# Optimization experiments

Hardware: AMD Instinct MI355X
Metric: run time of the kernel (lower is better)

The kernel has to match this reference:

```python
import jax, jax.numpy as jnp
import numpy as np

DIM_IN = 1024
DIM_Q = 1024
DIM_K = 1024
DIM_V = 1024
HEADS = 16

def setup_inputs() -> dict:
    key = jax.random.key(0)
    ks = jax.random.split(key, 5)
    s = 1.0 / np.sqrt(DIM_IN)
    return {
        "x": jax.random.normal(ks[0], (2, 2048, DIM_IN), dtype=jnp.float32),
        "Wq": jax.random.uniform(ks[1], (DIM_IN, DIM_Q), jnp.float32, -s, s),
        "Wk": jax.random.uniform(ks[2], (DIM_IN, DIM_K), jnp.float32, -s, s),
        "Wv": jax.random.uniform(ks[3], (DIM_IN, DIM_V), jnp.float32, -s, s),
        "Wo": jax.random.uniform(ks[4], (DIM_V, DIM_V), jnp.float32, -1.0/np.sqrt(DIM_V), 1.0/np.sqrt(DIM_V)),
    }

def reference(x, Wq, Wk, Wv, Wo):
    B, S, _ = x.shape
    H = HEADS
    q = (x @ Wq).reshape(B, S, H, DIM_Q // H).transpose(0, 2, 1, 3)  # [B,H,S,dq]
    k = (x @ Wk).reshape(B, S, H, DIM_K // H).transpose(0, 2, 1, 3)
    v = (x @ Wv).reshape(B, S, H, DIM_V // H).transpose(0, 2, 1, 3)
    scores = jnp.einsum("bhsd,bhtd->bhst", q, k)  # no pre-softmax scaling (as in source)
    # NOTE: source divides by sqrt(dim_q) AFTER softmax — replicated faithfully.
    attn = jax.nn.softmax(scores, axis=-1) / jnp.sqrt(jnp.float32(DIM_Q))
    out = jnp.einsum("bhst,bhtd->bhsd", attn, v)  # [B,H,S,dv]
    out = out.transpose(0, 2, 1, 3).reshape(B, S, DIM_V)
    return out @ Wo
```

## Files before the change

### kernel.cpp

```cpp
#include <hip/hip_runtime.h>
#include <hip/hip_bf16.h>


typedef __attribute__((ext_vector_type(8))) short bf16x8;
typedef __attribute__((ext_vector_type(4))) short short4v;
typedef __attribute__((ext_vector_type(4))) float f32x4;

typedef const __attribute__((address_space(1))) void gvoid_t;
typedef __attribute__((address_space(3))) void svoid_t;
#define GLDS16(g, l) \
  __builtin_amdgcn_global_load_lds((gvoid_t*)(g), (svoid_t*)(l), 16, 0, 0)

#define MFMA16(a, b, c) __builtin_amdgcn_mfma_f32_16x16x32_bf16((a), (b), (c), 0, 0, 0)

#if defined(__has_builtin)
#if __has_builtin(__builtin_amdgcn_exp2f)
#define EXP2(x) __builtin_amdgcn_exp2f(x)
#else
#define EXP2(x) exp2f(x)
#endif
#else
#define EXP2(x) exp2f(x)
#endif

#define LOG2E 1.4426950408889634f
#define NSHIFT 17.312340490667561f

static __device__ __forceinline__ short f2bf(float f) {
  __hip_bfloat16 h = __float2bfloat16(f);
  short s;
  __builtin_memcpy(&s, &h, 2);
  return s;
}

static __device__ __forceinline__ unsigned pack2bf(float lo, float hi) {
  float2 t; t.x = lo; t.y = hi;
  __hip_bfloat162 h2 = __float22bfloat162_rn(t);
  unsigned u;
  __builtin_memcpy(&u, &h2, 4);
  return u;
}

__global__ __launch_bounds__(256) void prep(const float* __restrict__ x,
                                            const float* __restrict__ Wq,
                                            const float* __restrict__ Wk,
                                            const float* __restrict__ Wv,
                                            const float* __restrict__ Wo,
                                            short* __restrict__ xb,
                                            short* __restrict__ wqkvt,
                                            short* __restrict__ wot) {
  __shared__ float tile[64][65];
  int bid = blockIdx.x;
  int tid = threadIdx.x;
  if (bid < 2048) {
    int i = bid * 256 + tid;
    const float4* p = (const float4*)(x + (size_t)i * 8);
    float4 a = p[0], b = p[1];
    bf16x8 o;
    o[0] = f2bf(a.x); o[1] = f2bf(a.y); o[2] = f2bf(a.z); o[3] = f2bf(a.w);
    o[4] = f2bf(b.x); o[5] = f2bf(b.y); o[6] = f2bf(b.z); o[7] = f2bf(b.w);
    *(bf16x8*)(xb + (size_t)i * 8) = o;
    return;
  }
  bid -= 2048;
  int mat = bid >> 8;
  int t = bid & 255;
  int tn = (t & 15) * 64;
  int tk = (t >> 4) * 64;
  const float* src = (mat == 0) ? Wq : (mat == 1) ? Wk : (mat == 2) ? Wv : Wo;
  short* dst = (mat < 3) ? (wqkvt + (size_t)mat * 1024 * 1024) : wot;

  int c4 = (tid & 15) * 4;
#pragma unroll
  for (int it = 0; it < 4; ++it) {
    int r = (tid >> 4) + it * 16;
    float4 v = *(const float4*)(src + (size_t)(tk + r) * 1024 + tn + c4);
    tile[r][c4 + 0] = v.x; tile[r][c4 + 1] = v.y;
    tile[r][c4 + 2] = v.z; tile[r][c4 + 3] = v.w;
  }
  __syncthreads();
  int n = tid >> 2;
  int kc = (tid & 3) * 16;
  bf16x8 o0, o1;
#pragma unroll
  for (int j = 0; j < 8; ++j) {
    o0[j] = f2bf(tile[kc + j][n]);
    o1[j] = f2bf(tile[kc + 8 + j][n]);
  }
  *(bf16x8*)(dst + (size_t)(tn + n) * 1024 + tk + kc) = o0;
  *(bf16x8*)(dst + (size_t)(tn + n) * 1024 + tk + kc + 8) = o1;
}

__global__ __launch_bounds__(256, 2) void gemm_qkv(const short* __restrict__ A,
                                                   const short* __restrict__ Bt,
                                                   short* __restrict__ qk,
                                                   short* __restrict__ vt) {
  constexpr int K = 1024;
  __shared__ short As[2][128 * 64];
  __shared__ short Bs[2][192 * 64];
  const int tid = threadIdx.x;
  const int lane = tid & 63;
  const int w = tid >> 6;
  const int lr = lane & 15, lg = lane >> 4;
  const int bid = blockIdx.x;
  const int orig = (bid & 7) * 64 + (bid >> 3);
  const int m0 = (orig >> 4) * 128, n0 = (orig & 15) * 192;
  const int wm = (w >> 1) * 64, wn = (w & 1) * 96;

  auto stage = [&](int kt, int bb) {
#pragma unroll
    for (int it = 0; it < 4; ++it) {
      int id = it * 256 + tid;
      int row = id >> 3, c = id & 7;
      int sc = c ^ (row & 7);
      GLDS16(A + (size_t)(m0 + row) * K + kt + sc * 8, &As[bb][0] + id * 8);
    }
#pragma unroll
    for (int it = 0; it < 6; ++it) {
      int id = it * 256 + tid;
      int row = id >> 3, c = id & 7;
      int sc = c ^ (row & 7);
      GLDS16(Bt + (size_t)(n0 + row) * K + kt + sc * 8, &Bs[bb][0] + id * 8);
    }
  };

  f32x4 acc[4][6] = {};

  stage(0, 0);
  __syncthreads();

  int cur = 0;
  for (int kt = 0; kt < K; kt += 64) {
    if (kt + 64 < K) stage(kt + 64, cur ^ 1);
    const short* Ab = &As[cur][0];
    const short* Bb = &Bs[cur][0];
#pragma unroll
    for (int kk2 = 0; kk2 < 2; ++kk2) {
      int cw = kk2 * 4 + lg;
      bf16x8 bfr[6];
#pragma unroll
      for (int ni = 0; ni < 6; ++ni) {
        int row = wn + ni * 16 + lr;
        bfr[ni] = *(const bf16x8*)(Bb + row * 64 + ((cw ^ (row & 7)) * 8));
      }
      __builtin_amdgcn_s_setprio(1);
#pragma unroll
      for (int mi = 0; mi < 4; ++mi) {
        int row = wm + mi * 16 + lr;
        bf16x8 af = *(const bf16x8*)(Ab + row * 64 + ((cw ^ (row & 7)) * 8));
#pragma unroll
        for (int ni = 0; ni < 6; ++ni)
          acc[mi][ni] = MFMA16(af, bfr[ni], acc[mi][ni]);
      }
      __builtin_amdgcn_s_setprio(0);
    }
    __syncthreads();
    cur ^= 1;
  }

#pragma unroll
  for (int mi = 0; mi < 4; ++mi) {
#pragma unroll
    for (int ni = 0; ni < 6; ++ni) {
      int m = m0 + wm + mi * 16 + lg * 4;
      int n = n0 + wn + ni * 16 + lr;
      if (n < 2048) {
        float sc = (n < 1024) ? LOG2E : 1.0f;
#pragma unroll
        for (int r = 0; r < 4; ++r)
          qk[(size_t)(m + r) * 2048 + n] = f2bf(acc[mi][ni][r] * sc);
      } else {
        int nv = n - 2048;
        int vtrow = ((m >> 11) * 16 + (nv >> 6)) * 64 + (nv & 63);
        int scol = m & 2047;
        int psc = (scol & ~31) | ((scol & 0xC) << 1) | ((scol & 16) >> 2) |
                  (scol & 3);
        short4v pv;
#pragma unroll
        for (int r = 0; r < 4; ++r) pv[r] = f2bf(acc[mi][ni][r]);
        *(short4v*)(vt + (size_t)vtrow * 2048 + psc) = pv;
      }
    }
  }
}

__global__ __launch_bounds__(256) void gemm_out(const short* __restrict__ A,
                                                const short* __restrict__ Bt,
                                                float* __restrict__ C) {
  constexpr int K = 1024, N = 1024;
  __shared__ short As[2][128 * 64];
  __shared__ short Bs[2][64 * 64];
  const int tid = threadIdx.x;
  const int lane = tid & 63;
  const int w = tid >> 6;
  const int lr = lane & 15, lg = lane >> 4;
  const int bid = blockIdx.x;
  const int orig = (bid & 7) * 64 + (bid >> 3);
  const int m0 = (orig >> 4) * 128, n0 = (orig & 15) * 64;
  const int wm = (w >> 1) * 64, wn = (w & 1) * 32;

  auto stage = [&](int kt, int bb) {
#pragma unroll
    for (int it = 0; it < 4; ++it) {
      int id = it * 256 + tid;
      int row = id >> 3, c = id & 7;
      int sc = c ^ (row & 7);
      GLDS16(A + (size_t)(m0 + row) * K + kt + sc * 8, &As[bb][0] + id * 8);
    }
#pragma unroll
    for (int it = 0; it < 2; ++it) {
      int id = it * 256 + tid;
      int row = id >> 3, c = id & 7;
      int sc = c ^ (row & 7);
      GLDS16(Bt + (size_t)(n0 + row) * K + kt + sc * 8, &Bs[bb][0] + id * 8);
    }
  };

  f32x4 acc[4][2] = {};

  stage(0, 0);
  __syncthreads();

  int cur = 0;
  for (int kt = 0; kt < K; kt += 64) {
    if (kt + 64 < K) stage(kt + 64, cur ^ 1);
    const short* Ab = &As[cur][0];
    const short* Bb = &Bs[cur][0];
#pragma unroll
    for (int kk2 = 0; kk2 < 2; ++kk2) {
      int cw = kk2 * 4 + lg;
      bf16x8 bfr[2];
#pragma unroll
      for (int ni = 0; ni < 2; ++ni) {
        int row = wn + ni * 16 + lr;
        bfr[ni] = *(const bf16x8*)(Bb + row * 64 + ((cw ^ (row & 7)) * 8));
      }
      __builtin_amdgcn_s_setprio(1);
#pragma unroll
      for (int mi = 0; mi < 4; ++mi) {
        int row = wm + mi * 16 + lr;
        bf16x8 af = *(const bf16x8*)(Ab + row * 64 + ((cw ^ (row & 7)) * 8));
#pragma unroll
        for (int ni = 0; ni < 2; ++ni)
          acc[mi][ni] = MFMA16(af, bfr[ni], acc[mi][ni]);
      }
      __builtin_amdgcn_s_setprio(0);
    }
    __syncthreads();
    cur ^= 1;
  }

#pragma unroll
  for (int mi = 0; mi < 4; ++mi) {
#pragma unroll
    for (int ni = 0; ni < 2; ++ni) {
      int m = m0 + wm + mi * 16 + lg * 4;
      int n = n0 + wn + ni * 16 + lr;
#pragma unroll
      for (int r = 0; r < 4; ++r) C[(size_t)(m + r) * N + n] = acc[mi][ni][r];
    }
  }
}

__global__ __launch_bounds__(256, 2) void attn_fwd(const short* __restrict__ qk,
                                                   const short* __restrict__ vt,
                                                   short* __restrict__ outb) {
  constexpr int S = 2048, LDQ = 2048;
  constexpr int NT = S / 128;
  const int fid = blockIdx.x;
  const int xcd = fid & 7, j = fid >> 3;
  const int qt = j & 15;
  const int pair = xcd * 4 + (j >> 4);
  const int h = pair & 15, b = pair >> 4;

  const int tid = threadIdx.x, lane = tid & 63, w = tid >> 6;
  const int lr = lane & 15, lg = lane >> 4;
  const int s7 = lr & 7;
  const int qb = qt * 128 + w * 32;

  __shared__ short Ks[2][128][64];
  __shared__ short Vs[2][64][128];

  const short* base = qk + (size_t)b * S * LDQ + h * 64;
  const short* vbase = vt + (size_t)(b * 16 + h) * 64 * 2048;

  bf16x8 qA0 = *(const bf16x8*)(base + (size_t)(qb + lr) * LDQ + lg * 8);
  bf16x8 qA1 = *(const bf16x8*)(base + (size_t)(qb + lr) * LDQ + 32 + lg * 8);
  bf16x8 qB0 = *(const bf16x8*)(base + (size_t)(qb + 16 + lr) * LDQ + lg * 8);
  bf16x8 qB1 = *(const bf16x8*)(base + (size_t)(qb + 16 + lr) * LDQ + 32 + lg * 8);

  bf16x8 ones;
#pragma unroll
  for (int i = 0; i < 8; ++i) ones[i] = (short)0x3F80;

  auto stageK = [&](int kt, int bb) {
#pragma unroll
    for (int it = 0; it < 4; ++it) {
      int id = it * 256 + tid;
      int row = id >> 3, c = id & 7;
      int sc = c ^ (row & 7);
      GLDS16(base + 1024 + (size_t)(kt + row) * LDQ + sc * 8,
             &Ks[bb][0][0] + id * 8);
    }
  };
  auto stageV = [&](int kt, int bb) {
#pragma unroll
    for (int it = 0; it < 4; ++it) {
      int id = it * 256 + tid;
      int row = id >> 4, c = id & 15;
      int sc = c ^ (row & 15);
      GLDS16(vbase + (size_t)row * 2048 + kt + sc * 8,
             &Vs[bb][0][0] + id * 8);
    }
  };

  f32x4 oA[4] = {}, oB[4] = {};
  f32x4 laccA = {}, laccB = {};
  bf16x8 pA[4], pB[4];

  stageK(0, 0);
  __syncthreads();

  for (int t = 0; t < NT; ++t) {
    const int cb = t & 1;
    if (t + 1 < NT) stageK((t + 1) * 128, cb ^ 1);
    stageV(t * 128, cb);

    const short* Kb = &Ks[cb][0][0];

    f32x4 sA[8], sB[8];
    __builtin_amdgcn_s_setprio(1);
#pragma unroll
    for (int kc = 0; kc < 8; ++kc) {
      int krow = kc * 16 + lr;
      bf16x8 kf0 = *(const bf16x8*)(Kb + krow * 64 + ((lg ^ s7) * 8));
      bf16x8 kf1 = *(const bf16x8*)(Kb + krow * 64 + (((4 + lg) ^ s7) * 8));
      f32x4 s = {-NSHIFT, -NSHIFT, -NSHIFT, -NSHIFT};
      s = MFMA16(kf0, qA0, s);
      s = MFMA16(kf1, qA1, s);
      sA[kc] = s;
      f32x4 u = {-NSHIFT, -NSHIFT, -NSHIFT, -NSHIFT};
      u = MFMA16(kf0, qB0, u);
      u = MFMA16(kf1, qB1, u);
      sB[kc] = u;
    }
    __builtin_amdgcn_s_setprio(0);

    if (t > 0) {
      const short* Vb = &Vs[cb ^ 1][0][0];
      __builtin_amdgcn_s_setprio(1);
#pragma unroll
      for (int g = 0; g < 4; ++g) {
        laccA = MFMA16(pA[g], ones, laccA);
        laccB = MFMA16(pB[g], ones, laccB);
      }
#pragma unroll
      for (int nc = 0; nc < 4; ++nc) {
        const short* vb = Vb + (nc * 16 + lr) * 128;
#pragma unroll
        for (int g = 0; g < 4; ++g) {
          bf16x8 vf = *(const bf16x8*)(vb + (((4 * g + lg) ^ lr) * 8));
          oA[nc] = MFMA16(pA[g], vf, oA[nc]);
          oB[nc] = MFMA16(pB[g], vf, oB[nc]);
        }
      }
      __builtin_amdgcn_s_setprio(0);
    }

    unsigned pwA[4][4], pwB[4][4];
#pragma unroll
    for (int kc = 0; kc < 8; ++kc) {
      {
        float p0 = EXP2(sA[kc][0]), p1 = EXP2(sA[kc][1]);
        float p2 = EXP2(sA[kc][2]), p3 = EXP2(sA[kc][3]);
        pwA[kc >> 1][(kc & 1) * 2 + 0] = pack2bf(p0, p1);
        pwA[kc >> 1][(kc & 1) * 2 + 1] = pack2bf(p2, p3);
      }
      {
        float p0 = EXP2(sB[kc][0]), p1 = EXP2(sB[kc][1]);
        float p2 = EXP2(sB[kc][2]), p3 = EXP2(sB[kc][3]);
        pwB[kc >> 1][(kc & 1) * 2 + 0] = pack2bf(p0, p1);
        pwB[kc >> 1][(kc & 1) * 2 + 1] = pack2bf(p2, p3);
      }
    }
#pragma unroll
    for (int g = 0; g < 4; ++g) {
      __builtin_memcpy(&pA[g], pwA[g], 16);
      __builtin_memcpy(&pB[g], pwB[g], 16);
    }

    __syncthreads();
  }

  {
    const short* Vb = &Vs[(NT - 1) & 1][0][0];
#pragma unroll
    for (int g = 0; g < 4; ++g) {
      laccA = MFMA16(pA[g], ones, laccA);
      laccB = MFMA16(pB[g], ones, laccB);
    }
#pragma unroll
    for (int nc = 0; nc < 4; ++nc) {
      const short* vb = Vb + (nc * 16 + lr) * 128;
#pragma unroll
      for (int g = 0; g < 4; ++g) {
        bf16x8 vf = *(const bf16x8*)(vb + (((4 * g + lg) ^ lr) * 8));
        oA[nc] = MFMA16(pA[g], vf, oA[nc]);
        oB[nc] = MFMA16(pB[g], vf, oB[nc]);
      }
    }
  }

#pragma unroll
  for (int r = 0; r < 4; ++r) {
    float dA = 1.0f / (laccA[r] * 32.0f);
    float dB = 1.0f / (laccB[r] * 32.0f);
#pragma unroll
    for (int nc = 0; nc < 4; ++nc) {
      int col = h * 64 + nc * 16 + lr;
      outb[(size_t)(b * S + qb + 4 * lg + r) * 1024 + col] = f2bf(oA[nc][r] * dA);
      outb[(size_t)(b * S + qb + 16 + 4 * lg + r) * 1024 + col] =
          f2bf(oB[nc][r] * dB);
    }
  }
}

extern "C" void kernel_launch(void* const* d_in, const int* in_sizes, int n_in,
                              void* d_out, int out_size, void* d_ws,
                              size_t ws_size, hipStream_t stream) {
  (void)in_sizes; (void)n_in; (void)out_size; (void)ws_size;
  const float* x = (const float*)d_in[0];
  const float* Wq = (const float*)d_in[1];
  const float* Wk = (const float*)d_in[2];
  const float* Wv = (const float*)d_in[3];
  const float* Wo = (const float*)d_in[4];

  char* p = (char*)d_ws;
  short* xb = (short*)p;      p += (size_t)4096 * 1024 * 2;
  short* wqkvt = (short*)p;   p += (size_t)3072 * 1024 * 2;
  short* wot = (short*)p;     p += (size_t)1024 * 1024 * 2;
  short* qk = (short*)p;      p += (size_t)4096 * 2048 * 2;
  short* vt = (short*)p;      p += (size_t)4096 * 1024 * 2;
  short* attno = (short*)p;   p += (size_t)4096 * 1024 * 2;

  prep<<<3072, 256, 0, stream>>>(x, Wq, Wk, Wv, Wo, xb, wqkvt, wot);
  gemm_qkv<<<512, 256, 0, stream>>>(xb, wqkvt, qk, vt);
  attn_fwd<<<512, 256, 0, stream>>>(qk, vt, attno);
  gemm_out<<<512, 256, 0, stream>>>(attno, wot, (float*)d_out);
}
```

Measured before the change: 99.75 us.

## Software-pipeline QK scores one tile ahead of softmax and PV in attention loop

Restructures the attention main loop so the QK^T MFMAs for tile t run in the same iteration as the exp/pack and PV MFMAs for tile t-1. Score buffers are ping-ponged across two register sets, and the loop is unrolled by two with explicit prologue and epilogue. The aim is to overlap the transcendental exp work with matrix-core work across tiles. In exchange it holds an extra set of score accumulators in registers, which raises register pressure and may reduce occupancy. The loop structure assumes NT is even.

```diff
diff --git a/kernel.cpp b/kernel.cpp
--- a/kernel.cpp
+++ b/kernel.cpp
@@ -316,19 +316,11 @@
 
   f32x4 oA[4] = {}, oB[4] = {};
   f32x4 laccA = {}, laccB = {};
-  bf16x8 pA[4], pB[4];
-
-  stageK(0, 0);
-  __syncthreads();
-
-  for (int t = 0; t < NT; ++t) {
+  f32x4 sXA[8], sXB[8], sYA[8], sYB[8];
+
+  auto qkStep = [&](int t, f32x4 (&swA)[8], f32x4 (&swB)[8]) {
     const int cb = t & 1;
-    if (t + 1 < NT) stageK((t + 1) * 128, cb ^ 1);
-    stageV(t * 128, cb);
-
     const short* Kb = &Ks[cb][0][0];
-
-    f32x4 sA[8], sB[8];
     __builtin_amdgcn_s_setprio(1);
 #pragma unroll
     for (int kc = 0; kc < 8; ++kc) {
@@ -338,62 +330,40 @@
       f32x4 s = {-NSHIFT, -NSHIFT, -NSHIFT, -NSHIFT};
       s = MFMA16(kf0, qA0, s);
       s = MFMA16(kf1, qA1, s);
-      sA[kc] = s;
+      swA[kc] = s;
       f32x4 u = {-NSHIFT, -NSHIFT, -NSHIFT, -NSHIFT};
       u = MFMA16(kf0, qB0, u);
       u = MFMA16(kf1, qB1, u);
-      sB[kc] = u;
+      swB[kc] = u;
     }
     __builtin_amdgcn_s_setprio(0);
-
-    if (t > 0) {
-      const short* Vb = &Vs[cb ^ 1][0][0];
-      __builtin_amdgcn_s_setprio(1);
-#pragma unroll
-      for (int g = 0; g < 4; ++g) {
-        laccA = MFMA16(pA[g], ones, laccA);
-        laccB = MFMA16(pB[g], ones, laccB);
-      }
-#pragma unroll
-      for (int nc = 0; nc < 4; ++nc) {
-        const short* vb = Vb + (nc * 16 + lr) * 128;
-#pragma unroll
-        for (int g = 0; g < 4; ++g) {
-          bf16x8 vf = *(const bf16x8*)(vb + (((4 * g + lg) ^ lr) * 8));
-          oA[nc] = MFMA16(pA[g], vf, oA[nc]);
-          oB[nc] = MFMA16(pB[g], vf, oB[nc]);
-        }
-      }
-      __builtin_amdgcn_s_setprio(0);
-    }
-
+  };
+
+  auto smPv = [&](f32x4 (&srA)[8], f32x4 (&srB)[8], int vb) {
     unsigned pwA[4][4], pwB[4][4];
 #pragma unroll
     for (int kc = 0; kc < 8; ++kc) {
       {
-        float p0 = EXP2(sA[kc][0]), p1 = EXP2(sA[kc][1]);
-        float p2 = EXP2(sA[kc][2]), p3 = EXP2(sA[kc][3]);
+        float p0 = EXP2(srA[kc][0]), p1 = EXP2(srA[kc][1]);
+        float p2 = EXP2(srA[kc][2]), p3 = EXP2(srA[kc][3]);
         pwA[kc >> 1][(kc & 1) * 2 + 0] = pack2bf(p0, p1);
         pwA[kc >> 1][(kc & 1) * 2 + 1] = pack2bf(p2, p3);
       }
       {
-        float p0 = EXP2(sB[kc][0]), p1 = EXP2(sB[kc][1]);
-        float p2 = EXP2(sB[kc][2]), p3 = EXP2(sB[kc][3]);
+        float p0 = EXP2(srB[kc][0]), p1 = EXP2(srB[kc][1]);
+        float p2 = EXP2(srB[kc][2]), p3 = EXP2(srB[kc][3]);
         pwB[kc >> 1][(kc & 1) * 2 + 0] = pack2bf(p0, p1);
         pwB[kc >> 1][(kc & 1) * 2 + 1] = pack2bf(p2, p3);
       }
     }
+    bf16x8 pA[4], pB[4];
 #pragma unroll
     for (int g = 0; g < 4; ++g) {
       __builtin_memcpy(&pA[g], pwA[g], 16);
       __builtin_memcpy(&pB[g], pwB[g], 16);
     }
-
-    __syncthreads();
-  }
-
-  {
-    const short* Vb = &Vs[(NT - 1) & 1][0][0];
+    const short* Vb = &Vs[vb][0][0];
+    __builtin_amdgcn_s_setprio(1);
 #pragma unroll
     for (int g = 0; g < 4; ++g) {
       laccA = MFMA16(pA[g], ones, laccA);
@@ -401,15 +371,52 @@
     }
 #pragma unroll
     for (int nc = 0; nc < 4; ++nc) {
-      const short* vb = Vb + (nc * 16 + lr) * 128;
+      const short* vb2 = Vb + (nc * 16 + lr) * 128;
 #pragma unroll
       for (int g = 0; g < 4; ++g) {
-        bf16x8 vf = *(const bf16x8*)(vb + (((4 * g + lg) ^ lr) * 8));
+        bf16x8 vf = *(const bf16x8*)(vb2 + (((4 * g + lg) ^ lr) * 8));
         oA[nc] = MFMA16(pA[g], vf, oA[nc]);
         oB[nc] = MFMA16(pB[g], vf, oB[nc]);
       }
     }
-  }
+    __builtin_amdgcn_s_setprio(0);
+  };
+
+  stageK(0, 0);
+  __syncthreads();
+
+  stageK(128, 1);
+  stageV(0, 0);
+  qkStep(0, sXA, sXB);
+  __syncthreads();
+
+  for (int tt = 1; tt + 1 < NT; tt += 2) {
+    {
+      const int t = tt, cb = t & 1;
+      stageK((t + 1) * 128, cb ^ 1);
+      stageV(t * 128, cb);
+      qkStep(t, sYA, sYB);
+      smPv(sXA, sXB, cb ^ 1);
+      __syncthreads();
+    }
+    {
+      const int t = tt + 1, cb = t & 1;
+      if (t + 1 < NT) stageK((t + 1) * 128, cb ^ 1);
+      stageV(t * 128, cb);
+      qkStep(t, sXA, sXB);
+      smPv(sYA, sYB, cb ^ 1);
+      __syncthreads();
+    }
+  }
+  {
+    const int t = NT - 1, cb = t & 1;
+    stageV(t * 128, cb);
+    qkStep(t, sYA, sYB);
+    smPv(sXA, sXB, cb ^ 1);
+    __syncthreads();
+  }
+
+  smPv(sYA, sYB, (NT - 1) & 1);
 
 #pragma unroll
   for (int r = 0; r < 4; ++r) {
```

Measured after the change: 103.0 us. 3.2% more time.
